# Kernel optimization log

Measured on AMD Instinct MI355X. Metric: run time of the kernel, lower is better.

The kernel has to match this reference:

```python
import jax, jax.numpy as jnp
import numpy as np
from jax import lax

EPS = 1e-5
K = 3  # DCN kernel size


def _conv(x, w, pad, lhs_dil=(1, 1)):
    return lax.conv_general_dilated(
        x, w, window_strides=(1, 1), padding=((pad, pad), (pad, pad)),
        lhs_dilation=lhs_dil, dimension_numbers=('NCHW', 'OIHW', 'NCHW'))


def _batchnorm(x, gamma, beta):
    # training-mode BN (batch statistics), matching nn.BatchNorm2d in train()
    m = jnp.mean(x, axis=(0, 2, 3), keepdims=True)
    v = jnp.var(x, axis=(0, 2, 3), keepdims=True)
    return (x - m) * lax.rsqrt(v + EPS) * gamma[None, :, None, None] + beta[None, :, None, None]


def _bilinear_sample(x, py, px):
    # x: [B,C,H,W]; py,px: [B,K2,H,W] fractional sample coords (zero-pad outside)
    B, C, H, W = x.shape
    K2 = py.shape[1]
    y0 = jnp.floor(py)
    x0 = jnp.floor(px)
    wy = (py - y0)[:, None]  # [B,1,K2,H,W]
    wx = (px - x0)[:, None]
    xf = x.reshape(B, C, H * W)

    def gather(yi, xi):
        valid = ((yi >= 0) & (yi <= H - 1) & (xi >= 0) & (xi <= W - 1)).astype(x.dtype)
        yc = jnp.clip(yi, 0, H - 1).astype(jnp.int32)
        xc = jnp.clip(xi, 0, W - 1).astype(jnp.int32)
        idx = (yc * W + xc).reshape(B, 1, -1)
        v = jnp.take_along_axis(xf, idx, axis=2).reshape(B, C, K2, H, W)
        return v * valid[:, None]

    v00 = gather(y0, x0)
    v01 = gather(y0, x0 + 1)
    v10 = gather(y0 + 1, x0)
    v11 = gather(y0 + 1, x0 + 1)
    return (v00 * (1 - wy) * (1 - wx) + v01 * (1 - wy) * wx
            + v10 * wy * (1 - wx) + v11 * wy * wx)  # [B,C,K2,H,W]


def _dcn(x, w_off, b_off, w_dcn, b_dcn):
    # Modulated deformable conv (DCNv2), stride 1, pad 1, dil 1, 1 deform group
    B, C, H, W = x.shape
    K2 = K * K
    om = _conv(x, w_off, pad=1) + b_off[None, :, None, None]  # [B,3*K2,H,W]
    dy, dx, m = om[:, :K2], om[:, K2:2 * K2], jax.nn.sigmoid(om[:, 2 * K2:])
    ki, kj = jnp.meshgrid(jnp.arange(K), jnp.arange(K), indexing='ij')
    ky = (ki.reshape(-1) - 1).astype(x.dtype)[None, :, None, None]
    kx = (kj.reshape(-1) - 1).astype(x.dtype)[None, :, None, None]
    py = dy + jnp.arange(H, dtype=x.dtype)[None, None, :, None] + ky
    px = dx + jnp.arange(W, dtype=x.dtype)[None, None, None, :] + kx
    val = _bilinear_sample(x, py, px) * m[:, None]  # [B,C,K2,H,W]
    Co = w_dcn.shape[0]
    out = jnp.einsum('bikhw,oik->bohw', val, w_dcn.reshape(Co, C, K2))
    return out + b_dcn[None, :, None, None]


def _conv_transpose(x, w_up):
    # torch ConvTranspose2d(k=4, stride=2, pad=1), weight [Cin, Cout, 4, 4]
    w = jnp.flip(w_up, axis=(2, 3)).transpose(1, 0, 2, 3)  # -> OIHW
    return _conv(x, w, pad=2, lhs_dil=(2, 2))


def setup_inputs() -> dict:
    key = jax.random.key(0)
    ks = jax.random.split(key, 8)
    B, Cin, Cout, H, W = 4, 256, 256, 64, 64
    x = jax.random.normal(ks[0], (B, Cin, H, W), dtype=jnp.float32)
    w_off = jax.random.normal(ks[1], (3 * K * K, Cin, K, K), dtype=jnp.float32) * 0.01
    b_off = jnp.zeros((3 * K * K,), dtype=jnp.float32)
    w_dcn = jax.random.normal(ks[2], (Cout, Cin, K, K), dtype=jnp.float32) * (1.0 / np.sqrt(Cin * K * K))
    b_dcn = jnp.zeros((Cout,), dtype=jnp.float32)
    gamma1 = jax.random.uniform(ks[3], (Cout,), dtype=jnp.float32, minval=0.5, maxval=1.5)
    beta1 = jax.random.normal(ks[4], (Cout,), dtype=jnp.float32) * 0.1
    w_up = jax.random.normal(ks[5], (Cout, Cout, 4, 4), dtype=jnp.float32) * (1.0 / np.sqrt(Cout * 16))
    gamma2 = jax.random.uniform(ks[6], (Cout,), dtype=jnp.float32, minval=0.5, maxval=1.5)
    beta2 = jax.random.normal(ks[7], (Cout,), dtype=jnp.float32) * 0.1
    return {'x': x, 'w_off': w_off, 'b_off': b_off, 'w_dcn': w_dcn, 'b_dcn': b_dcn,
            'gamma1': gamma1, 'beta1': beta1, 'w_up': w_up, 'gamma2': gamma2, 'beta2': beta2}


def reference(x, w_off, b_off, w_dcn, b_dcn, gamma1, beta1, w_up, gamma2, beta2):
    out = _dcn(x, w_off, b_off, w_dcn, b_dcn)
    out = jax.nn.relu(_batchnorm(out, gamma1, beta1))
    out = _conv_transpose(out, w_up)
    out = jax.nn.relu(_batchnorm(out, gamma2, beta2))
    return out
```

## Files before the change

### kernel.cpp

```cpp
#include <hip/hip_runtime.h>
#include <hip/hip_bf16.h>
#include <math.h>

#define B_   4
#define CIN  256
#define COUT 256
#define HW   4096

typedef __attribute__((ext_vector_type(8))) short short8;
typedef __attribute__((ext_vector_type(4))) float float4v;

#define LSTR  40
#define LSTR2 72
#define LSTR4 136

__device__ __forceinline__ float sigmoidf_(float v){ return 1.0f/(1.0f+expf(-v)); }
__device__ __forceinline__ ushort f2bf(float f){
  union { float f; unsigned u; } x; x.f = f;
  unsigned r = x.u + 0x7fffu + ((x.u>>16)&1u);
  return (ushort)(r>>16);
}
__device__ __forceinline__ float bflo(unsigned u){ union{unsigned u; float f;} c; c.u = u<<16;          return c.f; }
__device__ __forceinline__ float bfhi(unsigned u){ union{unsigned u; float f;} c; c.u = u & 0xffff0000u; return c.f; }

__global__ void k_transpose_x(const float* __restrict__ x, ushort* __restrict__ xtb){
  __shared__ float ts[32][33];
  int tx = threadIdx.x & 31, ty = threadIdx.x >> 5;
  int p0 = blockIdx.x * 32, c0 = blockIdx.y * 32, b = blockIdx.z;
  const float* xb = x + (size_t)b*CIN*HW;
#pragma unroll
  for(int q=0;q<4;q++){
    int c = ty + q*8;
    ts[c][tx] = xb[(size_t)(c0+c)*HW + p0+tx];
  }
  __syncthreads();
#pragma unroll
  for(int q=0;q<4;q++){
    int pr = ty + q*8;
    xtb[((size_t)(b*HW + p0+pr)<<8) + c0+tx] = f2bf(ts[tx][pr]);
  }
}

__global__ void k_build_all(const float* __restrict__ w_off, const float* __restrict__ w_dcn,
                            const float* __restrict__ w_up,
                            ushort* __restrict__ Wob, ushort* __restrict__ Wdb,
                            ushort* __restrict__ WT2c){
  int bid = blockIdx.x;
  if(bid < 288){
    int f = bid*256 + threadIdx.x;
    int kc = f>>10, o = (f>>5)&31, kk = f&31;
    int k = kc*32 + kk, tap = k>>8, c = k&255;
    float v = (o < 27) ? w_off[(size_t)o*2304 + c*9 + tap] : 0.f;
    Wob[f] = f2bf(v);
  } else if(bid < 288+2304){
    int f = (bid-288)*256 + threadIdx.x;
    int kc = f>>13, o = (f>>5)&255, kk = f&31;
    int k = kc>>3, c = ((kc&7)<<5) | kk;
    Wdb[f] = f2bf(w_dcn[(size_t)o*2304 + c*9 + k]);
  } else {
    int f = (bid-2592)*256 + threadIdx.x;
    int pp = f>>18, kc = (f>>13)&31, o = (f>>5)&255, kk = f&31;
    int k = kc*32 + kk, ab = k>>8, c = k&255;
    int a = ab>>1, bb = ab&1, ph = pp>>1, pw = pp&1;
    WT2c[f] = f2bf(w_up[(size_t)(c*COUT+o)*16 + (3-ph-2*a)*4 + (3-pw-2*bb)]);
  }
}

__global__ __launch_bounds__(256) void k_offset_mfma(const ushort* __restrict__ xtb,
                        const ushort* __restrict__ Wob, float* __restrict__ om){
  __shared__ ushort Vs[2][64*LSTR4];
  __shared__ int sIdx[576];
  int tid = threadIdx.x;
  int fb  = blockIdx.x + (blockIdx.y<<6);
  int b   = (fb&7)>>1;
  int px0 = ((((fb>>3)<<1) | (fb&1))) << 6;
  for(int t=tid; t<576; t+=256){
    int tap = t>>6, px = t&63;
    int p = px0+px, hh = p>>6, ww = p&63;
    int ih = hh + tap/3 - 1, iw = ww + tap%3 - 1;
    sIdx[t] = (ih>=0 && ih<64 && iw>=0 && iw<64) ? ((b*HW + ih*64+iw)<<8) : -1;
  }
  __syncthreads();

  int lane = tid&63, wv = tid>>6, lo = lane&15, hi = lane>>4;
  float4v acc[2];
  acc[0] = acc[1] = (float4v){0.f,0.f,0.f,0.f};
  int vpx = tid>>2, vseg = tid&3;
  const int wlane = lo*32 + hi*8;

#define OFF_WLOAD_ALLQ(Q, W) do{ \
    _Pragma("unroll") \
    for(int c_=0;c_<4;c_++){ \
      const ushort* wp_ = Wob + (((Q)*4+c_)<<10) + wlane; \
      W[2*c_+0] = *(const short8*)(wp_); \
      W[2*c_+1] = *(const short8*)(wp_ + 512); \
    } \
  }while(0)

#define OFF_GATHER_Q(Q, V) do{ \
    int k_ = (Q)>>1, c0_ = ((Q)&1)<<7; \
    int idx_ = sIdx[(k_<<6)+vpx]; \
    int coff_ = c0_ + (vseg<<5); \
    V[0]=make_uint4(0,0,0,0); V[1]=make_uint4(0,0,0,0); \
    V[2]=make_uint4(0,0,0,0); V[3]=make_uint4(0,0,0,0); \
    if(idx_ >= 0){ \
      V[0] = *(const uint4*)(xtb + idx_ + coff_); \
      V[1] = *(const uint4*)(xtb + idx_ + coff_ + 8); \
      V[2] = *(const uint4*)(xtb + idx_ + coff_ + 16); \
      V[3] = *(const uint4*)(xtb + idx_ + coff_ + 24); \
    } \
  }while(0)

#define OFF_VWRITE_Q(V, BUF) do{ \
    ushort* vp_ = &Vs[BUF][vpx*LSTR4 + (vseg<<5)]; \
    *(uint4*)(vp_)      = V[0]; \
    *(uint4*)(vp_ + 8)  = V[1]; \
    *(uint4*)(vp_ + 16) = V[2]; \
    *(uint4*)(vp_ + 24) = V[3]; \
  }while(0)

#define OFF_COMPUTE_Q2(W, BUF) do{ \
    const ushort* bp_ = &Vs[BUF][(wv*16+lo)*LSTR4 + hi*8]; \
    _Pragma("unroll") \
    for(int c_=0;c_<4;c_++){ \
      short8 ba_ = *(const short8*)(bp_ + c_*32); \
      acc[0] = __builtin_amdgcn_mfma_f32_16x16x32_bf16(W[2*c_+0], ba_, acc[0], 0,0,0); \
      acc[1] = __builtin_amdgcn_mfma_f32_16x16x32_bf16(W[2*c_+1], ba_, acc[1], 0,0,0); \
    } \
  }while(0)

  short8 w[8];
  uint4 vE[4], vO[4];
  OFF_GATHER_Q(0, vE);
  OFF_VWRITE_Q(vE, 0);
  OFF_GATHER_Q(1, vO);
  __syncthreads();

#pragma unroll 1
  for(int pb=0; pb<18; pb+=2){
    {
      OFF_WLOAD_ALLQ(pb, w);
      if(pb<16) OFF_GATHER_Q(pb+2, vE);
      OFF_COMPUTE_Q2(w, 0);
      OFF_VWRITE_Q(vO, 1);
      __syncthreads();
    }
    {
      OFF_WLOAD_ALLQ(pb+1, w);
      if(pb<15) OFF_GATHER_Q(pb+3, vO);
      OFF_COMPUTE_Q2(w, 1);
      if(pb<16) OFF_VWRITE_Q(vE, 0);
      __syncthreads();
    }
  }
  int p = px0 + wv*16 + lo;
#pragma unroll
  for(int mi=0;mi<2;mi++){
    int ob = mi*16 + hi*4;
    float4v a = (mi==0) ? acc[0] : acc[1];
#pragma unroll
    for(int r=0;r<4;r++){
      int o = ob + r;
      if(o < 27) om[(size_t)(b*27+o)*HW + p] = a[r];
    }
  }
}

#define DCN_WLOAD_ALLQ(Q, W) do{ \
    _Pragma("unroll") \
    for(int c_=0;c_<4;c_++){ \
      const ushort* wp_ = Wdb + ((size_t)((Q)*4+c_)<<13) + wlane; \
      W[4*c_+0] = *(const short8*)(wp_); \
      W[4*c_+1] = *(const short8*)(wp_ + 512); \
      W[4*c_+2] = *(const short8*)(wp_ + 1024); \
      W[4*c_+3] = *(const short8*)(wp_ + 1536); \
    } \
  }while(0)

#define DCN_GATHER_Q(Q, C, CF) do{ \
    int k_ = (Q)>>1, c0_ = ((Q)&1)<<7; \
    int t_ = (k_<<6) + vpx; \
    int pk_ = sPk[t_]; CF = sCf[t_]; \
    int coff_ = c0_ + (vseg<<4); \
    int iy0_=pk_&63, iy1_=(pk_>>6)&63, ix0_=(pk_>>12)&63, ix1_=(pk_>>18)&63; \
    const ushort* p00_ = xtb + cbase + (((iy0_<<6)+ix0_)<<8) + coff_; \
    const ushort* p01_ = xtb + cbase + (((iy0_<<6)+ix1_)<<8) + coff_; \
    const ushort* p10_ = xtb + cbase + (((iy1_<<6)+ix0_)<<8) + coff_; \
    const ushort* p11_ = xtb + cbase + (((iy1_<<6)+ix1_)<<8) + coff_; \
    C[0] = *(const uint4*)(p00_);     C[4] = *(const uint4*)(p00_ + 8); \
    C[1] = *(const uint4*)(p01_);     C[5] = *(const uint4*)(p01_ + 8); \
    C[2] = *(const uint4*)(p10_);     C[6] = *(const uint4*)(p10_ + 8); \
    C[3] = *(const uint4*)(p11_);     C[7] = *(const uint4*)(p11_ + 8); \
  }while(0)

#define DCN_BLEND_H(C0,C1,C2,C3, CF, DST) do{ \
    union{ ushort us[8]; uint4 q; } rr_; \
    rr_.us[0] = f2bf(CF.x*bflo(C0.x)+CF.y*bflo(C1.x)+CF.z*bflo(C2.x)+CF.w*bflo(C3.x)); \
    rr_.us[1] = f2bf(CF.x*bfhi(C0.x)+CF.y*bfhi(C1.x)+CF.z*bfhi(C2.x)+CF.w*bfhi(C3.x)); \
    rr_.us[2] = f2bf(CF.x*bflo(C0.y)+CF.y*bflo(C1.y)+CF.z*bflo(C2.y)+CF.w*bflo(C3.y)); \
    rr_.us[3] = f2bf(CF.x*bfhi(C0.y)+CF.y*bfhi(C1.y)+CF.z*bfhi(C2.y)+CF.w*bfhi(C3.y)); \
    rr_.us[4] = f2bf(CF.x*bflo(C0.z)+CF.y*bflo(C1.z)+CF.z*bflo(C2.z)+CF.w*bflo(C3.z)); \
    rr_.us[5] = f2bf(CF.x*bfhi(C0.z)+CF.y*bfhi(C1.z)+CF.z*bfhi(C2.z)+CF.w*bfhi(C3.z)); \
    rr_.us[6] = f2bf(CF.x*bflo(C0.w)+CF.y*bflo(C1.w)+CF.z*bflo(C2.w)+CF.w*bflo(C3.w)); \
    rr_.us[7] = f2bf(CF.x*bfhi(C0.w)+CF.y*bfhi(C1.w)+CF.z*bfhi(C2.w)+CF.w*bfhi(C3.w)); \
    *(uint4*)(DST) = rr_.q; \
  }while(0)

#define DCN_BLEND_Q(C, CF, BUF) do{ \
    ushort* dp_ = &Vs[BUF][vpx*LSTR4 + (vseg<<4)]; \
    DCN_BLEND_H(C[0],C[1],C[2],C[3], CF, dp_); \
    DCN_BLEND_H(C[4],C[5],C[6],C[7], CF, dp_ + 8); \
  }while(0)

#define DCN_COMPUTE_Q2(W, BUF) do{ \
    const ushort* bp_ = &Vs[BUF][(pn0+lo)*LSTR4 + hi*8]; \
    _Pragma("unroll") \
    for(int c_=0;c_<4;c_++){ \
      short8 b0_ = *(const short8*)(bp_ + c_*32); \
      short8 b1_ = *(const short8*)(bp_ + c_*32 + 16*LSTR4); \
      acc[0][0] = __builtin_amdgcn_mfma_f32_16x16x32_bf16(W[4*c_+0], b0_, acc[0][0], 0,0,0); \
      acc[0][1] = __builtin_amdgcn_mfma_f32_16x16x32_bf16(W[4*c_+0], b1_, acc[0][1], 0,0,0); \
      acc[1][0] = __builtin_amdgcn_mfma_f32_16x16x32_bf16(W[4*c_+1], b0_, acc[1][0], 0,0,0); \
      acc[1][1] = __builtin_amdgcn_mfma_f32_16x16x32_bf16(W[4*c_+1], b1_, acc[1][1], 0,0,0); \
      acc[2][0] = __builtin_amdgcn_mfma_f32_16x16x32_bf16(W[4*c_+2], b0_, acc[2][0], 0,0,0); \
      acc[2][1] = __builtin_amdgcn_mfma_f32_16x16x32_bf16(W[4*c_+2], b1_, acc[2][1], 0,0,0); \
      acc[3][0] = __builtin_amdgcn_mfma_f32_16x16x32_bf16(W[4*c_+3], b0_, acc[3][0], 0,0,0); \
      acc[3][1] = __builtin_amdgcn_mfma_f32_16x16x32_bf16(W[4*c_+3], b1_, acc[3][1], 0,0,0); \
    } \
  }while(0)

__global__ __launch_bounds__(512) void k_dcn_mfma(const ushort* __restrict__ xtb,
                        const float* __restrict__ om, const float* __restrict__ b_off,
                        const ushort* __restrict__ Wdb, float* __restrict__ out1){
  __shared__ ushort Vs[2][64*LSTR4];
  __shared__ int    sPk[576];
  __shared__ float4 sCf[576];
  int tid = threadIdx.x;
  int fb  = blockIdx.x + (blockIdx.y<<6);
  int b   = (fb&7)>>1;
  int px0 = ((((fb>>3)<<1) | (fb&1))) << 6;

  for(int t=tid; t<576; t+=512){
    int k = t>>6, px = t&63;
    int p = px0 + px, hh = p>>6, ww = p&63;
    const float* omp = om + (size_t)b*27*HW + p;
    float dy = omp[(size_t)k*HW]      + b_off[k];
    float dx = omp[(size_t)(9+k)*HW]  + b_off[9+k];
    float mo = sigmoidf_(omp[(size_t)(18+k)*HW] + b_off[18+k]);
    float py  = dy + (float)(hh + k/3 - 1);
    float pxf = dx + (float)(ww + k%3 - 1);
    float y0 = floorf(py), x0 = floorf(pxf);
    float wy = py - y0, wx = pxf - x0;
    float y1 = y0 + 1.0f, x1 = x0 + 1.0f;
    bool vy0 = (y0>=0.f)&&(y0<=63.f), vy1 = (y1>=0.f)&&(y1<=63.f);
    bool vx0 = (x0>=0.f)&&(x0<=63.f), vx1 = (x1>=0.f)&&(x1<=63.f);
    int iy0 = (int)fminf(fmaxf(y0,0.f),63.f);
    int iy1 = (int)fminf(fmaxf(y1,0.f),63.f);
    int ix0 = (int)fminf(fmaxf(x0,0.f),63.f);
    int ix1 = (int)fminf(fmaxf(x1,0.f),63.f);
    sPk[t] = iy0 | (iy1<<6) | (ix0<<12) | (ix1<<18);
    sCf[t] = make_float4((vy0&&vx0)? (1.f-wy)*(1.f-wx)*mo : 0.f,
                         (vy0&&vx1)? (1.f-wy)*wx*mo       : 0.f,
                         (vy1&&vx0)? wy*(1.f-wx)*mo       : 0.f,
                         (vy1&&vx1)? wy*wx*mo             : 0.f);
  }
  __syncthreads();

  int lane = tid&63, wv = tid>>6, lo = lane&15, hi = lane>>4;
  int om0 = (wv>>1)*64, pn0 = (wv&1)*32;
  float4v acc[4][2];
#pragma unroll
  for(int i=0;i<4;i++)
#pragma unroll
    for(int j=0;j<2;j++) acc[i][j] = (float4v){0.f,0.f,0.f,0.f};
  int cbase = (b*HW)<<8;
  int vpx = tid>>3, vseg = tid&7;
  const int wlane = (om0+lo)*32 + hi*8;

  short8 w[16];
  uint4 cE[8], cO[8];
  float4 fE, fO;

  DCN_GATHER_Q(0, cE, fE);
  DCN_BLEND_Q(cE, fE, 0);
  DCN_GATHER_Q(1, cO, fO);
  __syncthreads();

#pragma unroll 1
  for(int pb=0; pb<18; pb+=2){
    {
      DCN_WLOAD_ALLQ(pb, w);
      if(pb<16) DCN_GATHER_Q(pb+2, cE, fE);
      DCN_COMPUTE_Q2(w, 0);
      DCN_BLEND_Q(cO, fO, 1);
      __syncthreads();
    }
    {
      DCN_WLOAD_ALLQ(pb+1, w);
      if(pb<15) DCN_GATHER_Q(pb+3, cO, fO);
      DCN_COMPUTE_Q2(w, 1);
      if(pb<16) DCN_BLEND_Q(cE, fE, 0);
      __syncthreads();
    }
  }

#pragma unroll
  for(int i=0;i<4;i++){
    int ob = om0 + i*16 + hi*4;
#pragma unroll
    for(int r=0;r<4;r++){
      int o = ob + r;
      float* op = out1 + (size_t)(b*COUT + o)*HW + px0 + pn0 + lo;
#pragma unroll
      for(int j=0;j<2;j++) op[j*16] = acc[i][j][r];
    }
  }
}

__global__ void k_bn_stats(const float* __restrict__ xin, float* __restrict__ stats, int per_b){
  int o = blockIdx.x, tid = threadIdx.x;
  float s=0.f, ss=0.f;
  for(int b=0;b<B_;b++){
    const float* p = xin + (size_t)(b*COUT+o)*per_b;
    for(int i=tid;i<per_b;i+=256){ float v = p[i]; s+=v; ss+=v*v; }
  }
  __shared__ float rs[256], rss[256];
  rs[tid]=s; rss[tid]=ss; __syncthreads();
  for(int st=128; st>0; st>>=1){
    if(tid<st){ rs[tid]+=rs[tid+st]; rss[tid]+=rss[tid+st]; }
    __syncthreads();
  }
  if(tid==0){
    float n = (float)(B_*per_b);
    float mean = rs[0]/n;
    float var  = rss[0]/n - mean*mean;
    stats[o*2] = mean; stats[o*2+1] = rsqrtf(var + 1e-5f);
  }
}

__global__ void k_bn_stats_ct(const ushort* __restrict__ ct, float* __restrict__ stats){
  int o = blockIdx.x, tid = threadIdx.x;
  float s=0.f, ss=0.f;
  for(int pl=0; pl<16; ++pl){
    const ushort* p = ct + (((size_t)(pl*256 + o))<<12);
    for(int i=tid*8; i<4096; i+=2048){
      uint4 v = *(const uint4*)(p + i);
      float f;
      f=bflo(v.x); s+=f; ss+=f*f;  f=bfhi(v.x); s+=f; ss+=f*f;
      f=bflo(v.y); s+=f; ss+=f*f;  f=bfhi(v.y); s+=f; ss+=f*f;
      f=bflo(v.z); s+=f; ss+=f*f;  f=bfhi(v.z); s+=f; ss+=f*f;
      f=bflo(v.w); s+=f; ss+=f*f;  f=bfhi(v.w); s+=f; ss+=f*f;
    }
  }
  __shared__ float rs[256], rss[256];
  rs[tid]=s; rss[tid]=ss; __syncthreads();
  for(int st=128; st>0; st>>=1){
    if(tid<st){ rs[tid]+=rs[tid+st]; rss[tid]+=rss[tid+st]; }
    __syncthreads();
  }
  if(tid==0){
    float n = (float)(16*4096);
    float mean = rs[0]/n;
    float var  = rss[0]/n - mean*mean;
    stats[o*2] = mean; stats[o*2+1] = rsqrtf(var + 1e-5f);
  }
}

__global__ void k_bn1_apply_t(const float* __restrict__ out1, const float* __restrict__ stats,
                              const float* __restrict__ gamma, const float* __restrict__ beta,
                              ushort* __restrict__ y1b){
  __shared__ float ts[32][33];
  int tx = threadIdx.x & 31, ty = threadIdx.x >> 5;
  int p0 = blockIdx.x*32, o0 = blockIdx.y*32, b = blockIdx.z;
#pragma unroll
  for(int q=0;q<4;q++){
    int oo = ty + q*8; int o = o0 + oo;
    float m = stats[o*2], rstd = stats[o*2+1];
    float scale = rstd * gamma[o];
    float shift = beta[o] - m * scale;
    float v = out1[(size_t)(b*COUT+o)*HW + p0+tx];
    ts[oo][tx] = fmaxf(v*scale + shift, 0.f);
  }
  __syncthreads();
#pragma unroll
  for(int q=0;q<4;q++){
    int pr = ty + q*8;
    y1b[((size_t)(b*HW + p0+pr)<<8) + o0+tx] = f2bf(ts[tx][pr]);
  }
}

__global__ __launch_bounds__(512) void k_convt_mfma(const ushort* __restrict__ y1b,
                        const ushort* __restrict__ WT2c,
                        ushort* __restrict__ ct){
  __shared__ ushort Vs[2][256*LSTR2];
  __shared__ int sIdx[1024];
  int tid = threadIdx.x;
  int fb  = blockIdx.x + (blockIdx.y<<4) + (blockIdx.z<<6);
  int jj = fb&7, rr2 = fb>>3;
  int b   = jj>>1;
  int pp  = ((rr2>>4)<<1) | (jj&1);
  int px0 = (rr2&15) << 8;
  int ph = pp>>1, pw = pp&1;

  for(int t=tid; t<1024; t+=512){
    int ab = t>>8, px = t&255;
    int a = ab>>1, bb = ab&1;
    int p = px0+px, r = p>>6, s = p&63;
    int ih = r + ph - 1 + a, iw = s + pw - 1 + bb;
    sIdx[t] = (ih>=0 && ih<64 && iw>=0 && iw<64) ? ((b*HW + ih*64+iw)<<8) : -1;
  }
  __syncthreads();

  int lane = tid&63, wv = tid>>6, lo = lane&15, hi = lane>>4;
  int om0 = (wv>>1)*64;
  int pn0 = (wv&1)*128;
  float4v acc[4][8];
#pragma unroll
  for(int i=0;i<4;i++)
#pragma unroll
    for(int j=0;j<8;j++) acc[i][j] = (float4v){0.f,0.f,0.f,0.f};

  const ushort* wbase = WT2c + ((size_t)pp<<18);
  const int wlaneb = (om0+lo)*32 + hi*8;
  int vpx = tid>>1, vseg = tid&1;
  uint4 vpre[4];

#define CT3_PREFETCH(PC) do{ \
    int kc0_ = (PC)*2; \
    int ab_ = kc0_>>3, c0_ = (kc0_&7)<<5; \
    int idx_ = sIdx[(ab_<<8) + vpx]; \
    int co_ = c0_ + vseg*32; \
    vpre[0]=make_uint4(0,0,0,0); vpre[1]=make_uint4(0,0,0,0); \
    vpre[2]=make_uint4(0,0,0,0); vpre[3]=make_uint4(0,0,0,0); \
    if(idx_ >= 0){ \
      vpre[0] = *(const uint4*)(y1b + idx_ + co_); \
      vpre[1] = *(const uint4*)(y1b + idx_ + co_ + 8); \
      vpre[2] = *(const uint4*)(y1b + idx_ + co_ + 16); \
      vpre[3] = *(const uint4*)(y1b + idx_ + co_ + 24); \
    } \
  }while(0)

#define CT3_WRITE(BUF) do{ \
    ushort* vp_ = &Vs[BUF][vpx*LSTR2 + vseg*32]; \
    *(uint4*)(vp_)      = vpre[0]; \
    *(uint4*)(vp_ + 8)  = vpre[1]; \
    *(uint4*)(vp_ + 16) = vpre[2]; \
    *(uint4*)(vp_ + 24) = vpre[3]; \
  }while(0)

  CT3_PREFETCH(0);
  CT3_WRITE(0);
  __syncthreads();

#pragma unroll 1
  for(int pc=0; pc<16; ++pc){
    int cur = pc&1;
    if(pc < 15) CT3_PREFETCH(pc+1);
#pragma unroll
    for(int c=0; c<2; ++c){
      const ushort* wp = wbase + ((size_t)(((pc<<1)|c))<<13) + wlaneb;
      const ushort* bp = &Vs[cur][(pn0+lo)*LSTR2 + c*32 + hi*8];
      short8 bfr[8];
#pragma unroll
      for(int j=0;j<8;j++) bfr[j] = *(const short8*)(bp + j*16*LSTR2);
#pragma unroll
      for(int i=0;i<4;i++){
        short8 afr = *(const short8*)(wp + i*512);
#pragma unroll
        for(int j=0;j<8;j++)
          acc[i][j] = __builtin_amdgcn_mfma_f32_16x16x32_bf16(afr, bfr[j], acc[i][j], 0,0,0);
      }
    }
    if(pc < 15) CT3_WRITE(cur^1);
    __syncthreads();
  }

  ushort* cb = ct + (((size_t)(pp*4 + b)*256)<<12);
#pragma unroll
  for(int i=0;i<4;i++){
#pragma unroll
    for(int r=0;r<4;r++){
      int o = om0 + i*16 + hi*4 + r;
      ushort* row = cb + ((size_t)o<<12) + px0 + pn0 + lo;
#pragma unroll
      for(int j=0;j<8;j++) row[j*16] = f2bf(acc[i][j][r]);
    }
  }
}

__global__ void k_bn2_apply(const ushort* __restrict__ ct, const float* __restrict__ stats,
                            const float* __restrict__ gamma, const float* __restrict__ beta,
                            float* __restrict__ out){
  int gid = blockIdx.x*256 + threadIdx.x;
  int e4 = gid<<2;
  int b = e4>>22, o = (e4>>14)&255, q = e4&16383;
  int H2 = q>>7, W2 = q&127;
  int r = H2>>1, ph = H2&1, s0 = W2>>1;
  size_t base0 = (((size_t)((ph*2)*4 + b)*256 + o)<<12) + r*64 + s0;
  unsigned u0 = *(const unsigned*)(ct + base0);
  unsigned u1 = *(const unsigned*)(ct + base0 + ((size_t)4<<20));
  float m = stats[o*2], rstd = stats[o*2+1];
  float sc = rstd * gamma[o];
  float sh = beta[o] - m * sc;
  float4 v;
  v.x = fmaxf(bflo(u0)*sc + sh, 0.f);
  v.y = fmaxf(bflo(u1)*sc + sh, 0.f);
  v.z = fmaxf(bfhi(u0)*sc + sh, 0.f);
  v.w = fmaxf(bfhi(u1)*sc + sh, 0.f);
  *(float4*)(out + e4) = v;
}

extern "C" void kernel_launch(void* const* d_in, const int* in_sizes, int n_in,
                              void* d_out, int out_size, void* d_ws, size_t ws_size,
                              hipStream_t stream){
  (void)in_sizes; (void)n_in; (void)out_size; (void)ws_size;
  const float* x     = (const float*)d_in[0];
  const float* w_off = (const float*)d_in[1];
  const float* b_off = (const float*)d_in[2];
  const float* w_dcn = (const float*)d_in[3];
  const float* gamma1= (const float*)d_in[5];
  const float* beta1 = (const float*)d_in[6];
  const float* w_up  = (const float*)d_in[7];
  const float* gamma2= (const float*)d_in[8];
  const float* beta2 = (const float*)d_in[9];
  float* out = (float*)d_out;

  float* ws   = (float*)d_ws;
  ushort* ct  = (ushort*)ws;
  float* om   = ws;
  ushort* xtb = (ushort*)(ws + 442368);
  float* out1 = ws + 442368 + 2097152;
  float* base2 = ws + 8388608;
  ushort* y1b  = (ushort*)base2;
  ushort* WT2c = (ushort*)(base2 + 2097152);
  ushort* Wdb  = (ushort*)(base2 + 2097152 + 524288);
  ushort* Wob  = (ushort*)(base2 + 2097152 + 524288 + 294912);
  float* st1   = base2 + 2097152 + 524288 + 294912 + 36864;
  float* st2   = st1 + 512;

  k_transpose_x <<<dim3(128,8,4), 256, 0, stream>>>(x, xtb);
  k_build_all   <<<6688, 256, 0, stream>>>(w_off, w_dcn, w_up, Wob, Wdb, WT2c);
  k_offset_mfma <<<dim3(64,4),  256, 0, stream>>>(xtb, Wob, om);
  k_dcn_mfma    <<<dim3(64,4),  512, 0, stream>>>(xtb, om, b_off, Wdb, out1);
  k_bn_stats    <<<256,  256, 0, stream>>>(out1, st1, 4096);
  k_bn1_apply_t <<<dim3(128,8,4), 256, 0, stream>>>(out1, st1, gamma1, beta1, y1b);
  k_convt_mfma  <<<dim3(16,4,4),  512, 0, stream>>>(y1b, WT2c, ct);
  k_bn_stats_ct <<<256,  256, 0, stream>>>(ct, st2);
  k_bn2_apply   <<<16384,256, 0, stream>>>(ct, st2, gamma2, beta2, out);
}
```

Before: 267.8 us.

## Halve pixel tile in offset and DCN kernels to double block count

The offset-conv and deformable-conv MFMA kernels now process 32 pixels per block instead of 64, and the grid doubles from 256 to 512 blocks to fill more compute units on the GPU. The offset kernel also splits output channels across waves, and the pipeline loop is simplified to a single gather-ahead per stage. Launch bounds now request higher occupancy. The cost is that each block reuses its weight loads over half as many pixels, so weight traffic roughly doubles.

```diff
diff --git a/kernel.cpp b/kernel.cpp
--- a/kernel.cpp
+++ b/kernel.cpp
@@ -66,16 +66,16 @@
   }
 }
 
-__global__ __launch_bounds__(256) void k_offset_mfma(const ushort* __restrict__ xtb,
+__global__ __launch_bounds__(256, 2) void k_offset_mfma(const ushort* __restrict__ xtb,
                         const ushort* __restrict__ Wob, float* __restrict__ om){
-  __shared__ ushort Vs[2][64*LSTR4];
-  __shared__ int sIdx[576];
+  __shared__ ushort Vs[2][32*LSTR4];
+  __shared__ int sIdx[288];
   int tid = threadIdx.x;
-  int fb  = blockIdx.x + (blockIdx.y<<6);
+  int fb  = blockIdx.x + (blockIdx.y<<7);
   int b   = (fb&7)>>1;
-  int px0 = ((((fb>>3)<<1) | (fb&1))) << 6;
-  for(int t=tid; t<576; t+=256){
-    int tap = t>>6, px = t&63;
+  int px0 = ((((fb>>3)<<1) | (fb&1))) << 5;
+  for(int t=tid; t<288; t+=256){
+    int tap = t>>5, px = t&31;
     int p = px0+px, hh = p>>6, ww = p&63;
     int ih = hh + tap/3 - 1, iw = ww + tap%3 - 1;
     sIdx[t] = (ih>=0 && ih<64 && iw>=0 && iw<64) ? ((b*HW + ih*64+iw)<<8) : -1;
@@ -83,86 +83,65 @@
   __syncthreads();
 
   int lane = tid&63, wv = tid>>6, lo = lane&15, hi = lane>>4;
-  float4v acc[2];
-  acc[0] = acc[1] = (float4v){0.f,0.f,0.f,0.f};
-  int vpx = tid>>2, vseg = tid&3;
-  const int wlane = lo*32 + hi*8;
-
-#define OFF_WLOAD_ALLQ(Q, W) do{ \
+  int mi  = wv&1;
+  int ph2 = wv>>1;
+  float4v acc = (float4v){0.f,0.f,0.f,0.f};
+  int vpx = tid>>3, vseg = tid&7;
+  const int wlane = (mi*16+lo)*32 + hi*8;
+
+#define OFF_WLOAD4(Q, W) do{ \
     _Pragma("unroll") \
-    for(int c_=0;c_<4;c_++){ \
-      const ushort* wp_ = Wob + (((Q)*4+c_)<<10) + wlane; \
-      W[2*c_+0] = *(const short8*)(wp_); \
-      W[2*c_+1] = *(const short8*)(wp_ + 512); \
-    } \
+    for(int c_=0;c_<4;c_++) \
+      W[c_] = *(const short8*)(Wob + (((Q)*4+c_)<<10) + wlane); \
   }while(0)
 
 #define OFF_GATHER_Q(Q, V) do{ \
     int k_ = (Q)>>1, c0_ = ((Q)&1)<<7; \
-    int idx_ = sIdx[(k_<<6)+vpx]; \
-    int coff_ = c0_ + (vseg<<5); \
+    int idx_ = sIdx[(k_<<5)+vpx]; \
+    int coff_ = c0_ + (vseg<<4); \
     V[0]=make_uint4(0,0,0,0); V[1]=make_uint4(0,0,0,0); \
-    V[2]=make_uint4(0,0,0,0); V[3]=make_uint4(0,0,0,0); \
     if(idx_ >= 0){ \
       V[0] = *(const uint4*)(xtb + idx_ + coff_); \
       V[1] = *(const uint4*)(xtb + idx_ + coff_ + 8); \
-      V[2] = *(const uint4*)(xtb + idx_ + coff_ + 16); \
-      V[3] = *(const uint4*)(xtb + idx_ + coff_ + 24); \
     } \
   }while(0)
 
 #define OFF_VWRITE_Q(V, BUF) do{ \
-    ushort* vp_ = &Vs[BUF][vpx*LSTR4 + (vseg<<5)]; \
-    *(uint4*)(vp_)      = V[0]; \
-    *(uint4*)(vp_ + 8)  = V[1]; \
-    *(uint4*)(vp_ + 16) = V[2]; \
-    *(uint4*)(vp_ + 24) = V[3]; \
-  }while(0)
-
-#define OFF_COMPUTE_Q2(W, BUF) do{ \
-    const ushort* bp_ = &Vs[BUF][(wv*16+lo)*LSTR4 + hi*8]; \
+    ushort* vp_ = &Vs[BUF][vpx*LSTR4 + (vseg<<4)]; \
+    *(uint4*)(vp_)     = V[0]; \
+    *(uint4*)(vp_ + 8) = V[1]; \
+  }while(0)
+
+#define OFF_COMPUTE_Q(W, BUF) do{ \
+    const ushort* bp_ = &Vs[BUF][(ph2*16+lo)*LSTR4 + hi*8]; \
     _Pragma("unroll") \
     for(int c_=0;c_<4;c_++){ \
       short8 ba_ = *(const short8*)(bp_ + c_*32); \
-      acc[0] = __builtin_amdgcn_mfma_f32_16x16x32_bf16(W[2*c_+0], ba_, acc[0], 0,0,0); \
-      acc[1] = __builtin_amdgcn_mfma_f32_16x16x32_bf16(W[2*c_+1], ba_, acc[1], 0,0,0); \
+      acc = __builtin_amdgcn_mfma_f32_16x16x32_bf16(W[c_], ba_, acc, 0,0,0); \
     } \
   }while(0)
 
-  short8 w[8];
-  uint4 vE[4], vO[4];
+  short8 w[4];
+  uint4 vE[2];
   OFF_GATHER_Q(0, vE);
   OFF_VWRITE_Q(vE, 0);
-  OFF_GATHER_Q(1, vO);
   __syncthreads();
 
 #pragma unroll 1
-  for(int pb=0; pb<18; pb+=2){
-    {
-      OFF_WLOAD_ALLQ(pb, w);
-      if(pb<16) OFF_GATHER_Q(pb+2, vE);
-      OFF_COMPUTE_Q2(w, 0);
-      OFF_VWRITE_Q(vO, 1);
-      __syncthreads();
-    }
-    {
-      OFF_WLOAD_ALLQ(pb+1, w);
-      if(pb<15) OFF_GATHER_Q(pb+3, vO);
-      OFF_COMPUTE_Q2(w, 1);
-      if(pb<16) OFF_VWRITE_Q(vE, 0);
-      __syncthreads();
-    }
-  }
-  int p = px0 + wv*16 + lo;
-#pragma unroll
-  for(int mi=0;mi<2;mi++){
-    int ob = mi*16 + hi*4;
-    float4v a = (mi==0) ? acc[0] : acc[1];
-#pragma unroll
-    for(int r=0;r<4;r++){
-      int o = ob + r;
-      if(o < 27) om[(size_t)(b*27+o)*HW + p] = a[r];
-    }
+  for(int pc=0; pc<18; ++pc){
+    int cur = pc&1;
+    OFF_WLOAD4(pc, w);
+    if(pc<17) OFF_GATHER_Q(pc+1, vE);
+    OFF_COMPUTE_Q(w, cur);
+    if(pc<17) OFF_VWRITE_Q(vE, cur^1);
+    __syncthreads();
+  }
+  int p = px0 + ph2*16 + lo;
+  int ob = mi*16 + hi*4;
+#pragma unroll
+  for(int r=0;r<4;r++){
+    int o = ob + r;
+    if(o < 27) om[(size_t)(b*27+o)*HW + p] = acc[r];
   }
 }
 
@@ -179,69 +158,54 @@
 
 #define DCN_GATHER_Q(Q, C, CF) do{ \
     int k_ = (Q)>>1, c0_ = ((Q)&1)<<7; \
-    int t_ = (k_<<6) + vpx; \
+    int t_ = (k_<<5) + vpx; \
     int pk_ = sPk[t_]; CF = sCf[t_]; \
-    int coff_ = c0_ + (vseg<<4); \
+    int coff_ = c0_ + (vseg<<3); \
     int iy0_=pk_&63, iy1_=(pk_>>6)&63, ix0_=(pk_>>12)&63, ix1_=(pk_>>18)&63; \
-    const ushort* p00_ = xtb + cbase + (((iy0_<<6)+ix0_)<<8) + coff_; \
-    const ushort* p01_ = xtb + cbase + (((iy0_<<6)+ix1_)<<8) + coff_; \
-    const ushort* p10_ = xtb + cbase + (((iy1_<<6)+ix0_)<<8) + coff_; \
-    const ushort* p11_ = xtb + cbase + (((iy1_<<6)+ix1_)<<8) + coff_; \
-    C[0] = *(const uint4*)(p00_);     C[4] = *(const uint4*)(p00_ + 8); \
-    C[1] = *(const uint4*)(p01_);     C[5] = *(const uint4*)(p01_ + 8); \
-    C[2] = *(const uint4*)(p10_);     C[6] = *(const uint4*)(p10_ + 8); \
-    C[3] = *(const uint4*)(p11_);     C[7] = *(const uint4*)(p11_ + 8); \
-  }while(0)
-
-#define DCN_BLEND_H(C0,C1,C2,C3, CF, DST) do{ \
+    C[0] = *(const uint4*)(xtb + cbase + (((iy0_<<6)+ix0_)<<8) + coff_); \
+    C[1] = *(const uint4*)(xtb + cbase + (((iy0_<<6)+ix1_)<<8) + coff_); \
+    C[2] = *(const uint4*)(xtb + cbase + (((iy1_<<6)+ix0_)<<8) + coff_); \
+    C[3] = *(const uint4*)(xtb + cbase + (((iy1_<<6)+ix1_)<<8) + coff_); \
+  }while(0)
+
+#define DCN_BLEND_Q(C, CF, BUF) do{ \
     union{ ushort us[8]; uint4 q; } rr_; \
-    rr_.us[0] = f2bf(CF.x*bflo(C0.x)+CF.y*bflo(C1.x)+CF.z*bflo(C2.x)+CF.w*bflo(C3.x)); \
-    rr_.us[1] = f2bf(CF.x*bfhi(C0.x)+CF.y*bfhi(C1.x)+CF.z*bfhi(C2.x)+CF.w*bfhi(C3.x)); \
-    rr_.us[2] = f2bf(CF.x*bflo(C0.y)+CF.y*bflo(C1.y)+CF.z*bflo(C2.y)+CF.w*bflo(C3.y)); \
-    rr_.us[3] = f2bf(CF.x*bfhi(C0.y)+CF.y*bfhi(C1.y)+CF.z*bfhi(C2.y)+CF.w*bfhi(C3.y)); \
-    rr_.us[4] = f2bf(CF.x*bflo(C0.z)+CF.y*bflo(C1.z)+CF.z*bflo(C2.z)+CF.w*bflo(C3.z)); \
-    rr_.us[5] = f2bf(CF.x*bfhi(C0.z)+CF.y*bfhi(C1.z)+CF.z*bfhi(C2.z)+CF.w*bfhi(C3.z)); \
-    rr_.us[6] = f2bf(CF.x*bflo(C0.w)+CF.y*bflo(C1.w)+CF.z*bflo(C2.w)+CF.w*bflo(C3.w)); \
-    rr_.us[7] = f2bf(CF.x*bfhi(C0.w)+CF.y*bfhi(C1.w)+CF.z*bfhi(C2.w)+CF.w*bfhi(C3.w)); \
-    *(uint4*)(DST) = rr_.q; \
-  }while(0)
-
-#define DCN_BLEND_Q(C, CF, BUF) do{ \
-    ushort* dp_ = &Vs[BUF][vpx*LSTR4 + (vseg<<4)]; \
-    DCN_BLEND_H(C[0],C[1],C[2],C[3], CF, dp_); \
-    DCN_BLEND_H(C[4],C[5],C[6],C[7], CF, dp_ + 8); \
-  }while(0)
-
-#define DCN_COMPUTE_Q2(W, BUF) do{ \
+    rr_.us[0] = f2bf(CF.x*bflo(C[0].x)+CF.y*bflo(C[1].x)+CF.z*bflo(C[2].x)+CF.w*bflo(C[3].x)); \
+    rr_.us[1] = f2bf(CF.x*bfhi(C[0].x)+CF.y*bfhi(C[1].x)+CF.z*bfhi(C[2].x)+CF.w*bfhi(C[3].x)); \
+    rr_.us[2] = f2bf(CF.x*bflo(C[0].y)+CF.y*bflo(C[1].y)+CF.z*bflo(C[2].y)+CF.w*bflo(C[3].y)); \
+    rr_.us[3] = f2bf(CF.x*bfhi(C[0].y)+CF.y*bfhi(C[1].y)+CF.z*bfhi(C[2].y)+CF.w*bfhi(C[3].y)); \
+    rr_.us[4] = f2bf(CF.x*bflo(C[0].z)+CF.y*bflo(C[1].z)+CF.z*bflo(C[2].z)+CF.w*bflo(C[3].z)); \
+    rr_.us[5] = f2bf(CF.x*bfhi(C[0].z)+CF.y*bfhi(C[1].z)+CF.z*bfhi(C[2].z)+CF.w*bfhi(C[3].z)); \
+    rr_.us[6] = f2bf(CF.x*bflo(C[0].w)+CF.y*bflo(C[1].w)+CF.z*bflo(C[2].w)+CF.w*bflo(C[3].w)); \
+    rr_.us[7] = f2bf(CF.x*bfhi(C[0].w)+CF.y*bfhi(C[1].w)+CF.z*bfhi(C[2].w)+CF.w*bfhi(C[3].w)); \
+    *(uint4*)(&Vs[BUF][vpx*LSTR4 + (vseg<<3)]) = rr_.q; \
+  }while(0)
+
+#define DCN_COMPUTE_Q(W, BUF) do{ \
     const ushort* bp_ = &Vs[BUF][(pn0+lo)*LSTR4 + hi*8]; \
     _Pragma("unroll") \
     for(int c_=0;c_<4;c_++){ \
       short8 b0_ = *(const short8*)(bp_ + c_*32); \
-      short8 b1_ = *(const short8*)(bp_ + c_*32 + 16*LSTR4); \
-      acc[0][0] = __builtin_amdgcn_mfma_f32_16x16x32_bf16(W[4*c_+0], b0_, acc[0][0], 0,0,0); \
-      acc[0][1] = __builtin_amdgcn_mfma_f32_16x16x32_bf16(W[4*c_+0], b1_, acc[0][1], 0,0,0); \
-      acc[1][0] = __builtin_amdgcn_mfma_f32_16x16x32_bf16(W[4*c_+1], b0_, acc[1][0], 0,0,0); \
-      acc[1][1] = __builtin_amdgcn_mfma_f32_16x16x32_bf16(W[4*c_+1], b1_, acc[1][1], 0,0,0); \
-      acc[2][0] = __builtin_amdgcn_mfma_f32_16x16x32_bf16(W[4*c_+2], b0_, acc[2][0], 0,0,0); \
-      acc[2][1] = __builtin_amdgcn_mfma_f32_16x16x32_bf16(W[4*c_+2], b1_, acc[2][1], 0,0,0); \
-      acc[3][0] = __builtin_amdgcn_mfma_f32_16x16x32_bf16(W[4*c_+3], b0_, acc[3][0], 0,0,0); \
-      acc[3][1] = __builtin_amdgcn_mfma_f32_16x16x32_bf16(W[4*c_+3], b1_, acc[3][1], 0,0,0); \
+      acc[0] = __builtin_amdgcn_mfma_f32_16x16x32_bf16(W[4*c_+0], b0_, acc[0], 0,0,0); \
+      acc[1] = __builtin_amdgcn_mfma_f32_16x16x32_bf16(W[4*c_+1], b0_, acc[1], 0,0,0); \
+      acc[2] = __builtin_amdgcn_mfma_f32_16x16x32_bf16(W[4*c_+2], b0_, acc[2], 0,0,0); \
+      acc[3] = __builtin_amdgcn_mfma_f32_16x16x32_bf16(W[4*c_+3], b0_, acc[3], 0,0,0); \
     } \
   }while(0)
 
-__global__ __launch_bounds__(512) void k_dcn_mfma(const ushort* __restrict__ xtb,
+__global__ __launch_bounds__(512, 4) void k_dcn_mfma(const ushort* __restrict__ xtb,
                         const float* __restrict__ om, const float* __restrict__ b_off,
                         const ushort* __restrict__ Wdb, float* __restrict__ out1){
-  __shared__ ushort Vs[2][64*LSTR4];
-  __shared__ int    sPk[576];
-  __shared__ float4 sCf[576];
+  __shared__ ushort Vs[2][32*LSTR4];
+  __shared__ int    sPk[288];
+  __shared__ float4 sCf[288];
   int tid = threadIdx.x;
-  int fb  = blockIdx.x + (blockIdx.y<<6);
+  int fb  = blockIdx.x + (blockIdx.y<<7);
   int b   = (fb&7)>>1;
-  int px0 = ((((fb>>3)<<1) | (fb&1))) << 6;
-
-  for(int t=tid; t<576; t+=512){
-    int k = t>>6, px = t&63;
+  int px0 = ((((fb>>3)<<1) | (fb&1))) << 5;
+
+  if(tid < 288){
+    int k = tid>>5, px = tid&31;
     int p = px0 + px, hh = p>>6, ww = p&63;
     const float* omp = om + (size_t)b*27*HW + p;
     float dy = omp[(size_t)k*HW]      + b_off[k];
@@ -258,50 +222,39 @@
     int iy1 = (int)fminf(fmaxf(y1,0.f),63.f);
     int ix0 = (int)fminf(fmaxf(x0,0.f),63.f);
     int ix1 = (int)fminf(fmaxf(x1,0.f),63.f);
-    sPk[t] = iy0 | (iy1<<6) | (ix0<<12) | (ix1<<18);
-    sCf[t] = make_float4((vy0&&vx0)? (1.f-wy)*(1.f-wx)*mo : 0.f,
-                         (vy0&&vx1)? (1.f-wy)*wx*mo       : 0.f,
-                         (vy1&&vx0)? wy*(1.f-wx)*mo       : 0.f,
-                         (vy1&&vx1)? wy*wx*mo             : 0.f);
+    sPk[tid] = iy0 | (iy1<<6) | (ix0<<12) | (ix1<<18);
+    sCf[tid] = make_float4((vy0&&vx0)? (1.f-wy)*(1.f-wx)*mo : 0.f,
+                           (vy0&&vx1)? (1.f-wy)*wx*mo       : 0.f,
+                           (vy1&&vx0)? wy*(1.f-wx)*mo       : 0.f,
+                           (vy1&&vx1)? wy*wx*mo             : 0.f);
   }
   __syncthreads();
 
   int lane = tid&63, wv = tid>>6, lo = lane&15, hi = lane>>4;
-  int om0 = (wv>>1)*64, pn0 = (wv&1)*32;
-  float4v acc[4][2];
-#pragma unroll
-  for(int i=0;i<4;i++)
-#pragma unroll
-    for(int j=0;j<2;j++) acc[i][j] = (float4v){0.f,0.f,0.f,0.f};
+  int om0 = (wv>>1)*64, pn0 = (wv&1)*16;
+  float4v acc[4];
+#pragma unroll
+  for(int i=0;i<4;i++) acc[i] = (float4v){0.f,0.f,0.f,0.f};
   int cbase = (b*HW)<<8;
-  int vpx = tid>>3, vseg = tid&7;
+  int vpx = tid>>4, vseg = tid&15;
   const int wlane = (om0+lo)*32 + hi*8;
 
   short8 w[16];
-  uint4 cE[8], cO[8];
-  float4 fE, fO;
+  uint4 cE[4];
+  float4 fE;
 
   DCN_GATHER_Q(0, cE, fE);
   DCN_BLEND_Q(cE, fE, 0);
-  DCN_GATHER_Q(1, cO, fO);
   __syncthreads();
 
 #pragma unroll 1
-  for(int pb=0; pb<18; pb+=2){
-    {
-      DCN_WLOAD_ALLQ(pb, w);
-      if(pb<16) DCN_GATHER_Q(pb+2, cE, fE);
-      DCN_COMPUTE_Q2(w, 0);
-      DCN_BLEND_Q(cO, fO, 1);
-      __syncthreads();
-    }
-    {
-      DCN_WLOAD_ALLQ(pb+1, w);
-      if(pb<15) DCN_GATHER_Q(pb+3, cO, fO);
-      DCN_COMPUTE_Q2(w, 1);
-      if(pb<16) DCN_BLEND_Q(cE, fE, 0);
-      __syncthreads();
-    }
+  for(int pc=0; pc<18; ++pc){
+    int cur = pc&1;
+    DCN_WLOAD_ALLQ(pc, w);
+    if(pc<17) DCN_GATHER_Q(pc+1, cE, fE);
+    DCN_COMPUTE_Q(w, cur);
+    if(pc<17) DCN_BLEND_Q(cE, fE, cur^1);
+    __syncthreads();
   }
 
 #pragma unroll
@@ -310,9 +263,7 @@
 #pragma unroll
     for(int r=0;r<4;r++){
       int o = ob + r;
-      float* op = out1 + (size_t)(b*COUT + o)*HW + px0 + pn0 + lo;
-#pragma unroll
-      for(int j=0;j<2;j++) op[j*16] = acc[i][j][r];
+      out1[(size_t)(b*COUT + o)*HW + px0 + pn0 + lo] = acc[i][r];
     }
   }
 }
@@ -540,8 +491,8 @@
 
   k_transpose_x <<<dim3(128,8,4), 256, 0, stream>>>(x, xtb);
   k_build_all   <<<6688, 256, 0, stream>>>(w_off, w_dcn, w_up, Wob, Wdb, WT2c);
-  k_offset_mfma <<<dim3(64,4),  256, 0, stream>>>(xtb, Wob, om);
-  k_dcn_mfma    <<<dim3(64,4),  512, 0, stream>>>(xtb, om, b_off, Wdb, out1);
+  k_offset_mfma <<<dim3(128,4),  256, 0, stream>>>(xtb, Wob, om);
+  k_dcn_mfma    <<<dim3(128,4),  512, 0, stream>>>(xtb, om, b_off, Wdb, out1);
   k_bn_stats    <<<256,  256, 0, stream>>>(out1, st1, 4096);
   k_bn1_apply_t <<<dim3(128,8,4), 256, 0, stream>>>(out1, st1, gamma1, beta1, y1b);
   k_convt_mfma  <<<dim3(16,4,4),  512, 0, stream>>>(y1b, WT2c, ct);
```

After: 287.5 us. +7.4%, slower.

## Split-K the offset and DCN GEMMs across two blocks, store partials in bf16

Applied to the files above, without the earlier changes.

The offset conv and DCN GEMM kernels now split the 18-step reduction across two z-blocks, doubling the grid from 256 to 512 blocks to fill more CUs. Each half writes its own partial; the DCN partials are stored as bf16 and summed later in the BN stats and BN apply kernels. This adds partial-buffer traffic and a bf16 rounding of each partial before summation. The prefetch buffer drops from double to single registers, which may reduce register pressure.

```diff
diff --git a/kernel.cpp b/kernel.cpp
--- a/kernel.cpp
+++ b/kernel.cpp
@@ -67,13 +67,14 @@
 }
 
 __global__ __launch_bounds__(256) void k_offset_mfma(const ushort* __restrict__ xtb,
-                        const ushort* __restrict__ Wob, float* __restrict__ om){
+                        const ushort* __restrict__ Wob, float* __restrict__ om2){
   __shared__ ushort Vs[2][64*LSTR4];
   __shared__ int sIdx[576];
   int tid = threadIdx.x;
   int fb  = blockIdx.x + (blockIdx.y<<6);
   int b   = (fb&7)>>1;
   int px0 = ((((fb>>3)<<1) | (fb&1))) << 6;
+  int z   = blockIdx.z;
   for(int t=tid; t<576; t+=256){
     int tap = t>>6, px = t&63;
     int p = px0+px, hh = p>>6, ww = p&63;
@@ -130,28 +131,20 @@
   }while(0)
 
   short8 w[8];
-  uint4 vE[4], vO[4];
-  OFF_GATHER_Q(0, vE);
+  uint4 vE[4];
+  OFF_GATHER_Q(z*9, vE);
   OFF_VWRITE_Q(vE, 0);
-  OFF_GATHER_Q(1, vO);
   __syncthreads();
 
 #pragma unroll 1
-  for(int pb=0; pb<18; pb+=2){
-    {
-      OFF_WLOAD_ALLQ(pb, w);
-      if(pb<16) OFF_GATHER_Q(pb+2, vE);
-      OFF_COMPUTE_Q2(w, 0);
-      OFF_VWRITE_Q(vO, 1);
-      __syncthreads();
-    }
-    {
-      OFF_WLOAD_ALLQ(pb+1, w);
-      if(pb<15) OFF_GATHER_Q(pb+3, vO);
-      OFF_COMPUTE_Q2(w, 1);
-      if(pb<16) OFF_VWRITE_Q(vE, 0);
-      __syncthreads();
-    }
+  for(int pc=0; pc<9; ++pc){
+    int cur = pc&1;
+    int q = z*9 + pc;
+    OFF_WLOAD_ALLQ(q, w);
+    if(pc<8) OFF_GATHER_Q(q+1, vE);
+    OFF_COMPUTE_Q2(w, cur);
+    if(pc<8) OFF_VWRITE_Q(vE, cur^1);
+    __syncthreads();
   }
   int p = px0 + wv*16 + lo;
 #pragma unroll
@@ -161,7 +154,7 @@
 #pragma unroll
     for(int r=0;r<4;r++){
       int o = ob + r;
-      if(o < 27) om[(size_t)(b*27+o)*HW + p] = a[r];
+      if(o < 27) om2[(size_t)((z*B_+b)*27+o)*HW + p] = a[r];
     }
   }
 }
@@ -230,8 +223,8 @@
   }while(0)
 
 __global__ __launch_bounds__(512) void k_dcn_mfma(const ushort* __restrict__ xtb,
-                        const float* __restrict__ om, const float* __restrict__ b_off,
-                        const ushort* __restrict__ Wdb, float* __restrict__ out1){
+                        const float* __restrict__ om2, const float* __restrict__ b_off,
+                        const ushort* __restrict__ Wdb, ushort* __restrict__ out1u){
   __shared__ ushort Vs[2][64*LSTR4];
   __shared__ int    sPk[576];
   __shared__ float4 sCf[576];
@@ -239,14 +232,16 @@
   int fb  = blockIdx.x + (blockIdx.y<<6);
   int b   = (fb&7)>>1;
   int px0 = ((((fb>>3)<<1) | (fb&1))) << 6;
+  int z   = blockIdx.z;
 
   for(int t=tid; t<576; t+=512){
     int k = t>>6, px = t&63;
     int p = px0 + px, hh = p>>6, ww = p&63;
-    const float* omp = om + (size_t)b*27*HW + p;
-    float dy = omp[(size_t)k*HW]      + b_off[k];
-    float dx = omp[(size_t)(9+k)*HW]  + b_off[9+k];
-    float mo = sigmoidf_(omp[(size_t)(18+k)*HW] + b_off[18+k]);
+    const float* oma = om2 + (size_t)b*27*HW + p;
+    const float* omb = oma + (size_t)B_*27*HW;
+    float dy = oma[(size_t)k*HW]      + omb[(size_t)k*HW]      + b_off[k];
+    float dx = oma[(size_t)(9+k)*HW]  + omb[(size_t)(9+k)*HW]  + b_off[9+k];
+    float mo = sigmoidf_(oma[(size_t)(18+k)*HW] + omb[(size_t)(18+k)*HW] + b_off[18+k]);
     float py  = dy + (float)(hh + k/3 - 1);
     float pxf = dx + (float)(ww + k%3 - 1);
     float y0 = floorf(py), x0 = floorf(pxf);
@@ -278,51 +273,53 @@
   const int wlane = (om0+lo)*32 + hi*8;
 
   short8 w[16];
-  uint4 cE[8], cO[8];
-  float4 fE, fO;
-
-  DCN_GATHER_Q(0, cE, fE);
+  uint4 cE[8];
+  float4 fE;
+
+  DCN_GATHER_Q(z*9, cE, fE);
   DCN_BLEND_Q(cE, fE, 0);
-  DCN_GATHER_Q(1, cO, fO);
   __syncthreads();
 
 #pragma unroll 1
-  for(int pb=0; pb<18; pb+=2){
-    {
-      DCN_WLOAD_ALLQ(pb, w);
-      if(pb<16) DCN_GATHER_Q(pb+2, cE, fE);
-      DCN_COMPUTE_Q2(w, 0);
-      DCN_BLEND_Q(cO, fO, 1);
-      __syncthreads();
-    }
-    {
-      DCN_WLOAD_ALLQ(pb+1, w);
-      if(pb<15) DCN_GATHER_Q(pb+3, cO, fO);
-      DCN_COMPUTE_Q2(w, 1);
-      if(pb<16) DCN_BLEND_Q(cE, fE, 0);
-      __syncthreads();
-    }
-  }
-
+  for(int pc=0; pc<9; ++pc){
+    int cur = pc&1;
+    int q = z*9 + pc;
+    DCN_WLOAD_ALLQ(q, w);
+    if(pc<8) DCN_GATHER_Q(q+1, cE, fE);
+    DCN_COMPUTE_Q2(w, cur);
+    if(pc<8) DCN_BLEND_Q(cE, fE, cur^1);
+    __syncthreads();
+  }
+
+  ushort* op0 = out1u + ((size_t)((z*B_+b)*COUT)<<12) + px0 + pn0 + lo;
 #pragma unroll
   for(int i=0;i<4;i++){
     int ob = om0 + i*16 + hi*4;
 #pragma unroll
     for(int r=0;r<4;r++){
       int o = ob + r;
-      float* op = out1 + (size_t)(b*COUT + o)*HW + px0 + pn0 + lo;
-#pragma unroll
-      for(int j=0;j<2;j++) op[j*16] = acc[i][j][r];
+      ushort* op = op0 + ((size_t)o<<12);
+#pragma unroll
+      for(int j=0;j<2;j++) op[j*16] = f2bf(acc[i][j][r]);
     }
   }
 }
 
-__global__ void k_bn_stats(const float* __restrict__ xin, float* __restrict__ stats, int per_b){
+__global__ void k_bn_stats_bf2(const ushort* __restrict__ out1u, float* __restrict__ stats){
   int o = blockIdx.x, tid = threadIdx.x;
   float s=0.f, ss=0.f;
   for(int b=0;b<B_;b++){
-    const float* p = xin + (size_t)(b*COUT+o)*per_b;
-    for(int i=tid;i<per_b;i+=256){ float v = p[i]; s+=v; ss+=v*v; }
+    const ushort* pa = out1u + ((size_t)(b*COUT+o)<<12);
+    const ushort* pb = pa + ((size_t)B_*COUT<<12);
+    for(int i=tid*8; i<4096; i+=2048){
+      uint4 va = *(const uint4*)(pa + i);
+      uint4 vb = *(const uint4*)(pb + i);
+      float f;
+      f=bflo(va.x)+bflo(vb.x); s+=f; ss+=f*f;  f=bfhi(va.x)+bfhi(vb.x); s+=f; ss+=f*f;
+      f=bflo(va.y)+bflo(vb.y); s+=f; ss+=f*f;  f=bfhi(va.y)+bfhi(vb.y); s+=f; ss+=f*f;
+      f=bflo(va.z)+bflo(vb.z); s+=f; ss+=f*f;  f=bfhi(va.z)+bfhi(vb.z); s+=f; ss+=f*f;
+      f=bflo(va.w)+bflo(vb.w); s+=f; ss+=f*f;  f=bfhi(va.w)+bfhi(vb.w); s+=f; ss+=f*f;
+    }
   }
   __shared__ float rs[256], rss[256];
   rs[tid]=s; rss[tid]=ss; __syncthreads();
@@ -331,7 +328,7 @@
     __syncthreads();
   }
   if(tid==0){
-    float n = (float)(B_*per_b);
+    float n = (float)(B_*HW);
     float mean = rs[0]/n;
     float var  = rss[0]/n - mean*mean;
     stats[o*2] = mean; stats[o*2+1] = rsqrtf(var + 1e-5f);
@@ -366,7 +363,7 @@
   }
 }
 
-__global__ void k_bn1_apply_t(const float* __restrict__ out1, const float* __restrict__ stats,
+__global__ void k_bn1_apply_t(const ushort* __restrict__ out1u, const float* __restrict__ stats,
                               const float* __restrict__ gamma, const float* __restrict__ beta,
                               ushort* __restrict__ y1b){
   __shared__ float ts[32][33];
@@ -378,7 +375,8 @@
     float m = stats[o*2], rstd = stats[o*2+1];
     float scale = rstd * gamma[o];
     float shift = beta[o] - m * scale;
-    float v = out1[(size_t)(b*COUT+o)*HW + p0+tx];
+    size_t idx = ((size_t)(b*COUT+o)<<12) + p0+tx;
+    float v = bflo((unsigned)out1u[idx]) + bflo((unsigned)out1u[idx + ((size_t)B_*COUT<<12)]);
     ts[oo][tx] = fmaxf(v*scale + shift, 0.f);
   }
   __syncthreads();
@@ -525,11 +523,11 @@
   const float* beta2 = (const float*)d_in[9];
   float* out = (float*)d_out;
 
-  float* ws   = (float*)d_ws;
-  ushort* ct  = (ushort*)ws;
-  float* om   = ws;
-  ushort* xtb = (ushort*)(ws + 442368);
-  float* out1 = ws + 442368 + 2097152;
+  float* ws    = (float*)d_ws;
+  ushort* ct   = (ushort*)ws;
+  float* om2   = ws;
+  ushort* xtb  = (ushort*)(ws + 884736);
+  ushort* out1u= (ushort*)(ws + 884736 + 2097152);
   float* base2 = ws + 8388608;
   ushort* y1b  = (ushort*)base2;
   ushort* WT2c = (ushort*)(base2 + 2097152);
@@ -540,10 +538,10 @@
 
   k_transpose_x <<<dim3(128,8,4), 256, 0, stream>>>(x, xtb);
   k_build_all   <<<6688, 256, 0, stream>>>(w_off, w_dcn, w_up, Wob, Wdb, WT2c);
-  k_offset_mfma <<<dim3(64,4),  256, 0, stream>>>(xtb, Wob, om);
-  k_dcn_mfma    <<<dim3(64,4),  512, 0, stream>>>(xtb, om, b_off, Wdb, out1);
-  k_bn_stats    <<<256,  256, 0, stream>>>(out1, st1, 4096);
-  k_bn1_apply_t <<<dim3(128,8,4), 256, 0, stream>>>(out1, st1, gamma1, beta1, y1b);
+  k_offset_mfma <<<dim3(64,4,2), 256, 0, stream>>>(xtb, Wob, om2);
+  k_dcn_mfma    <<<dim3(64,4,2), 512, 0, stream>>>(xtb, om2, b_off, Wdb, out1u);
+  k_bn_stats_bf2<<<256,  256, 0, stream>>>(out1u, st1);
+  k_bn1_apply_t <<<dim3(128,8,4), 256, 0, stream>>>(out1u, st1, gamma1, beta1, y1b);
   k_convt_mfma  <<<dim3(16,4,4),  512, 0, stream>>>(y1b, WT2c, ct);
   k_bn_stats_ct <<<256,  256, 0, stream>>>(ct, st2);
   k_bn2_apply   <<<16384,256, 0, stream>>>(ct, st2, gamma2, beta2, out);
```

New measurement: 257.6 us. 1.04x faster.
